# Kernel optimization log

Hardware: AMD Instinct MI355X
Metric: run time of the kernel (lower is better)

Reference implementation:

```python
import jax, jax.numpy as jnp
import numpy as np

K_FUTURE = 3
GAMMA = 0.25
LAMBDA_CP = 0.1
EPS = 1e-08


def setup_inputs() -> dict:
    key = jax.random.key(0)
    ks = jax.random.split(key, 8)
    B, T, d, Kc = 64, 512, 1024, 256
    Z = jax.random.normal(ks[0], (B, T, d), dtype=jnp.float32)
    # torch init: uniform(-1/Kc, 1/Kc)
    codebook = jax.random.uniform(ks[1], (Kc, d), dtype=jnp.float32,
                                  minval=-1.0 / Kc, maxval=1.0 / Kc)
    s = 1.0 / np.sqrt(d)
    gru_Wih = jax.random.normal(ks[2], (3 * d, d), dtype=jnp.float32) * s
    gru_Whh = jax.random.normal(ks[3], (3 * d, d), dtype=jnp.float32) * s
    gru_bih = jnp.zeros((3 * d,), jnp.float32)
    gru_bhh = jnp.zeros((3 * d,), jnp.float32)
    proj_W = jax.random.normal(ks[4], (d, d), dtype=jnp.float32) * s
    proj_b = jnp.zeros((d,), jnp.float32)
    return {"Z": Z, "codebook": codebook, "gru_Wih": gru_Wih, "gru_Whh": gru_Whh,
            "gru_bih": gru_bih, "gru_bhh": gru_bhh, "proj_W": proj_W, "proj_b": proj_b}


def _gru(x, Wih, Whh, bih, bhh):
    # x: (B, T, d) -> hidden states (B, T, d); torch GRU gate math
    B, T, d = x.shape

    def step(h, xt):
        gi = xt @ Wih.T + bih
        gh = h @ Whh.T + bhh
        i_r, i_z, i_n = jnp.split(gi, 3, axis=-1)
        h_r, h_z, h_n = jnp.split(gh, 3, axis=-1)
        r = jax.nn.sigmoid(i_r + h_r)
        z = jax.nn.sigmoid(i_z + h_z)
        n = jnp.tanh(i_n + r * h_n)
        h_new = (1.0 - z) * n + z * h
        return h_new, h_new

    h0 = jnp.zeros((B, d), x.dtype)
    _, hs = jax.lax.scan(step, h0, jnp.swapaxes(x, 0, 1))
    return jnp.swapaxes(hs, 0, 1)


def _quantize(Z, codebook):
    B, T, d = Z.shape
    flat = Z.reshape(-1, d)                                   # (N, d)
    # squared euclidean distances; argmin identical to cdist(p=2)
    d2 = (jnp.sum(flat * flat, axis=1, keepdims=True)
          - 2.0 * flat @ codebook.T
          + jnp.sum(codebook * codebook, axis=1)[None, :])    # (N, Kc)
    idx = jnp.argmin(d2, axis=1)                              # (N,)
    quantized = codebook[idx].reshape(B, T, d)
    return quantized, idx.reshape(B, T)


def _context_loss(Z, quantized, gru_Wih, gru_Whh, gru_bih, gru_bhh, proj_W, proj_b):
    B, T, d = Z.shape
    hs = _gru(quantized, gru_Wih, gru_Whh, gru_bih, gru_bhh)
    h = hs @ proj_W.T + proj_b                                # (B, T, d)
    total = jnp.float32(0.0)
    for k in range(1, K_FUTURE + 1):
        if T <= k:
            continue
        hk = h[:, :T - k]                                     # (B, T-k, d)
        zk = Z[:, k:]                                         # (B, T-k, d)
        pos = jnp.einsum('btd,btd->bt', hk, zk)               # (B, T-k)
        # sum over tau of mean over batch
        pos_loss = jnp.sum(jnp.mean(-jnp.log(jax.nn.sigmoid(pos) + EPS), axis=0))
        # negatives use a random batch permutation; the mean over (b, c) is
        # permutation-invariant, so compute the full pairwise logits.
        neg = jnp.einsum('btd,ctd->tbc', hk, zk)              # (T-k, B, B)
        neg_loss = jnp.sum(jnp.mean(-jnp.log(1.0 - jax.nn.sigmoid(neg) + EPS), axis=(1, 2)))
        total = total + pos_loss + LAMBDA_CP * neg_loss
    if K_FUTURE > 0 and T > K_FUTURE:
        total = total / (K_FUTURE * (T - K_FUTURE))
    return total


def _vq_loss(Z, quantized):
    commitment = jnp.mean((jax.lax.stop_gradient(Z) - quantized) ** 2)
    codebook_l = jnp.mean((Z - jax.lax.stop_gradient(quantized)) ** 2)
    return commitment + GAMMA * codebook_l


def reference(Z, codebook, gru_Wih, gru_Whh, gru_bih, gru_bhh, proj_W, proj_b):
    quantized, indices = _quantize(Z, codebook)
    L_cp = _context_loss(Z, quantized, gru_Wih, gru_Whh, gru_bih, gru_bhh, proj_W, proj_b)
    L_vq = _vq_loss(Z, quantized)
    L_total = L_cp + L_vq
    return quantized, indices, L_total, L_cp, L_vq
```

## Files before the change

### kernel.cpp

```cpp
#include <hip/hip_runtime.h>
#include <hip/hip_bf16.h>

#define B_ 64
#define T_ 512
#define D_ 1024
#define NQ_ (B_*T_*D_)
#define NI_ (B_*T_)

typedef __attribute__((ext_vector_type(8))) short bf16x8;
typedef __attribute__((ext_vector_type(4))) float f32x4;

__device__ inline ushort f2bf(float f) {
    uint x = __float_as_uint(f);
    return (ushort)((x + 0x7FFFu + ((x >> 16) & 1u)) >> 16);
}
__device__ inline float bf2f(ushort u) { return __uint_as_float(((uint)u) << 16); }

__device__ __forceinline__ void astore(ushort* p, ushort v) {
    __hip_atomic_store(p, v, __ATOMIC_RELAXED, __HIP_MEMORY_SCOPE_AGENT);
}

typedef const __attribute__((address_space(1))) void GV;
typedef __attribute__((address_space(3))) void LV;
__device__ __forceinline__ void gll16(const void* g, void* l) {
    __builtin_amdgcn_global_load_lds((GV*)g, (LV*)l, 16, 0, 0);
}

__device__ __forceinline__ float sigf(float x) { return 1.0f / (1.0f + __expf(-x)); }
__device__ __forceinline__ float tanhfast(float x) {
    float e = __expf(-2.0f * fabsf(x));
    float t = (1.0f - e) / (1.0f + e);
    return copysignf(t, x);
}

__global__ __launch_bounds__(256) void conv_kernel(const float* __restrict__ src,
                                                   ushort* __restrict__ dst, int n) {
    int i = (blockIdx.x * 256 + threadIdx.x) * 4;
    if (i >= n) return;
    float4 v = *reinterpret_cast<const float4*>(src + i);
    ushort4 o;
    o.x = f2bf(v.x); o.y = f2bf(v.y); o.z = f2bf(v.z); o.w = f2bf(v.w);
    *reinterpret_cast<ushort4*>(dst + i) = o;
}

__global__ __launch_bounds__(256) void whhfr_kernel(const float* __restrict__ Whh,
                                                    ushort* __restrict__ Whh_fr) {
    int l = threadIdx.x & 63;
    int unit = blockIdx.x * 4 + (threadIdx.x >> 6);
    int c = unit & 31;
    int g = (unit >> 5) % 3;
    int jb = unit / 96;
    int row = g * 1024 + jb * 16 + (l & 15);
    int k0 = c * 32 + (l >> 4) * 8;
    const float* s = Whh + (size_t)row * 1024 + k0;
    float4 f0 = *reinterpret_cast<const float4*>(s);
    float4 f1 = *reinterpret_cast<const float4*>(s + 4);
    uint4 pk;
    pk.x = (uint)f2bf(f0.x) | ((uint)f2bf(f0.y) << 16);
    pk.y = (uint)f2bf(f0.z) | ((uint)f2bf(f0.w) << 16);
    pk.z = (uint)f2bf(f1.x) | ((uint)f2bf(f1.y) << 16);
    pk.w = (uint)f2bf(f1.z) | ((uint)f2bf(f1.w) << 16);
    reinterpret_cast<uint4*>(Whh_fr)[(size_t)unit * 64 + l] = pk;
}

__device__ inline float np_pairwise_sq_1024(const float* a) {
    float L[8];
    for (int c = 0; c < 8; ++c) {
        const float* p = a + c * 128;
        float r[8];
        #pragma unroll
        for (int k = 0; k < 8; ++k) r[k] = __fmul_rn(p[k], p[k]);
        for (int i = 8; i < 128; i += 8) {
            #pragma unroll
            for (int k = 0; k < 8; ++k) {
                float v = p[i + k];
                r[k] = __fadd_rn(r[k], __fmul_rn(v, v));
            }
        }
        L[c] = __fadd_rn(__fadd_rn(__fadd_rn(r[0], r[1]), __fadd_rn(r[2], r[3])),
                         __fadd_rn(__fadd_rn(r[4], r[5]), __fadd_rn(r[6], r[7])));
    }
    return __fadd_rn(__fadd_rn(__fadd_rn(L[0], L[1]), __fadd_rn(L[2], L[3])),
                     __fadd_rn(__fadd_rn(L[4], L[5]), __fadd_rn(L[6], L[7])));
}

__global__ __launch_bounds__(256) void c2_kernel(const float* __restrict__ cb,
                                                 float* __restrict__ c2) {
    int j = threadIdx.x;
    c2[j] = np_pairwise_sq_1024(cb + (size_t)j * D_);
}

__global__ __launch_bounds__(256) void quantize_kernel(const float* __restrict__ Z,
                                                       const float* __restrict__ cb,
                                                       const float* __restrict__ c2,
                                                       float* __restrict__ qout,
                                                       float* __restrict__ idxout,
                                                       int* __restrict__ idxT) {
    __shared__ float rows[8][D_];
    __shared__ float z2s[8];
    __shared__ float d2s[256];
    __shared__ int   idxs[256];
    __shared__ int   bestIdx[8];
    int tid = threadIdx.x;
    size_t row0 = (size_t)blockIdx.x * 8;

    for (int p = 0; p < 8; ++p) {
        float4 v = *reinterpret_cast<const float4*>(Z + (row0 + p) * D_ + tid * 4);
        *reinterpret_cast<float4*>(&rows[p][tid * 4]) = v;
    }
    __syncthreads();

    if (tid < 8) z2s[tid] = np_pairwise_sq_1024(rows[tid]);

    float g2[8];
    #pragma unroll
    for (int r = 0; r < 8; ++r) g2[r] = 0.0f;
    const float* crow = cb + (size_t)tid * D_;
    for (int e = 0; e < D_; e += 4) {
        float4 cv = *reinterpret_cast<const float4*>(crow + e);
        #pragma unroll
        for (int r = 0; r < 8; ++r) {
            g2[r] = __fmaf_rn(__fmul_rn(2.0f, rows[r][e]),     cv.x, g2[r]);
            g2[r] = __fmaf_rn(__fmul_rn(2.0f, rows[r][e + 1]), cv.y, g2[r]);
            g2[r] = __fmaf_rn(__fmul_rn(2.0f, rows[r][e + 2]), cv.z, g2[r]);
            g2[r] = __fmaf_rn(__fmul_rn(2.0f, rows[r][e + 3]), cv.w, g2[r]);
        }
    }
    __syncthreads();

    for (int r = 0; r < 8; ++r) {
        d2s[tid] = __fadd_rn(__fsub_rn(z2s[r], g2[r]), c2[tid]);
        idxs[tid] = tid;
        __syncthreads();
        for (int s = 128; s > 0; s >>= 1) {
            if (tid < s) {
                float ov = d2s[tid + s]; int oi = idxs[tid + s];
                if (ov < d2s[tid] || (ov == d2s[tid] && oi < idxs[tid])) {
                    d2s[tid] = ov; idxs[tid] = oi;
                }
            }
            __syncthreads();
        }
        if (tid == 0) bestIdx[r] = idxs[0];
        __syncthreads();
    }

    if (tid < 8) {
        int row = (int)row0 + tid;
        idxout[row] = (float)bestIdx[tid];
        idxT[((row & 511) << 6) + (row >> 9)] = bestIdx[tid];
    }
    for (int r = 0; r < 8; ++r) {
        int bi = bestIdx[r];
        float4 v = *reinterpret_cast<const float4*>(cb + (size_t)bi * D_ + tid * 4);
        *reinterpret_cast<float4*>(qout + (row0 + r) * D_ + tid * 4) = v;
    }
}

__global__ __launch_bounds__(256) void gmat_kernel(const float* __restrict__ cb,
                                                   const float* __restrict__ Wih,
                                                   const float* __restrict__ bih,
                                                   const float* __restrict__ bhh,
                                                   ushort* __restrict__ Gp) {
    int m0 = blockIdx.x * 64;
    int n0 = blockIdx.y * 64;
    __shared__ ushort As[64][136];
    __shared__ ushort Bs[64][136];
    int tid = threadIdx.x;
    int w = tid >> 6, l = tid & 63, lr = l & 15, lk = l >> 4;
    f32x4 acc[4];
    #pragma unroll
    for (int i = 0; i < 4; ++i) acc[i] = f32x4{0.f, 0.f, 0.f, 0.f};

    for (int kc = 0; kc < D_; kc += 128) {
        for (int v = tid; v < 2048; v += 256) {
            int r = (v >> 4) & 63, kp = (v & 15) << 3;
            const float* src = (v < 1024) ? (cb  + (size_t)(m0 + r) * D_ + kc + kp)
                                          : (Wih + (size_t)(n0 + r) * D_ + kc + kp);
            float4 f0 = *reinterpret_cast<const float4*>(src);
            float4 f1 = *reinterpret_cast<const float4*>(src + 4);
            uint4 pk;
            pk.x = (uint)f2bf(f0.x) | ((uint)f2bf(f0.y) << 16);
            pk.y = (uint)f2bf(f0.z) | ((uint)f2bf(f0.w) << 16);
            pk.z = (uint)f2bf(f1.x) | ((uint)f2bf(f1.y) << 16);
            pk.w = (uint)f2bf(f1.z) | ((uint)f2bf(f1.w) << 16);
            ushort* dst = (v < 1024) ? &As[r][kp] : &Bs[r][kp];
            *reinterpret_cast<uint4*>(dst) = pk;
        }
        __syncthreads();
        #pragma unroll
        for (int kk = 0; kk < 4; ++kk) {
            bf16x8 bb = *reinterpret_cast<const bf16x8*>(&Bs[(w << 4) + lr][(kk << 5) + (lk << 3)]);
            #pragma unroll
            for (int mi = 0; mi < 4; ++mi) {
                bf16x8 a = *reinterpret_cast<const bf16x8*>(&As[(mi << 4) + lr][(kk << 5) + (lk << 3)]);
                acc[mi] = __builtin_amdgcn_mfma_f32_16x16x32_bf16(a, bb, acc[mi], 0, 0, 0);
            }
        }
        __syncthreads();
    }
    int n = n0 + (w << 4) + lr;
    int gate = n >> 10, jj = n & 1023;
    float bias = bih[n] + (gate < 2 ? bhh[n] : 0.0f);
    #pragma unroll
    for (int mi = 0; mi < 4; ++mi)
        #pragma unroll
        for (int reg = 0; reg < 4; ++reg) {
            int m = m0 + (mi << 4) + (lk << 2) + reg;
            Gp[((((size_t)m << 10) | jj) << 2) + gate] = f2bf(acc[mi][reg] + bias);
        }
}

__global__ __launch_bounds__(256, 1) void recur_kernel(
    const ushort* __restrict__ Whh_fr,
    const ushort* __restrict__ Gp,
    const int*    __restrict__ idxT,
    const float*  __restrict__ bhh,
    ushort* h_hist,
    uint*   flags)
{
    extern __shared__ ushort dynlds[];
    const int tid = threadIdx.x, blk = blockIdx.x;
    const int w = tid >> 6, l = tid & 63;
    const int lr = l & 15, lk = l >> 4;
    const int j0 = blk << 4, j = j0 + lr;
    const int b_base = (w << 4) + (lk << 2);
    const float bhhn = bhh[2048 + j];
    const ushort* Bbase = Whh_fr + (size_t)blk * 49152;
    ushort* myfrag = dynlds + (w << 14);
    const int rowoff = (((w << 4) + lr) << 10) + (lk << 3);
    float hfp[4] = {0.f, 0.f, 0.f, 0.f};
    bool dead = false;

    bf16x8 Bfr[96];
    #pragma unroll
    for (int c = 0; c < 32; ++c) {
        Bfr[c]      = *reinterpret_cast<const bf16x8*>(Bbase +         (c << 9) + (l << 3));
        Bfr[32 + c] = *reinterpret_cast<const bf16x8*>(Bbase + 16384 + (c << 9) + (l << 3));
        Bfr[64 + c] = *reinterpret_cast<const bf16x8*>(Bbase + 32768 + (c << 9) + (l << 3));
    }

    for (int t = 0; t < T_; ++t) {
        const ushort* src = h_hist + ((size_t)(t == 0 ? 512 : t - 1) << 16) + rowoff;
        #pragma unroll
        for (int c = 0; c < 32; ++c)
            gll16(src + (c << 5), myfrag + (c << 9));
        __syncthreads();

        f32x4 acc0 = {0.f,0.f,0.f,0.f}, acc1 = acc0, acc2 = acc0;
        #pragma unroll
        for (int c = 0; c < 32; ++c) {
            bf16x8 a = *reinterpret_cast<const bf16x8*>(myfrag + (c << 9) + (l << 3));
            acc0 = __builtin_amdgcn_mfma_f32_16x16x32_bf16(a, Bfr[c],      acc0, 0, 0, 0);
            acc1 = __builtin_amdgcn_mfma_f32_16x16x32_bf16(a, Bfr[32 + c], acc1, 0, 0, 0);
            acc2 = __builtin_amdgcn_mfma_f32_16x16x32_bf16(a, Bfr[64 + c], acc2, 0, 0, 0);
        }

        ushort* hw = h_hist + ((size_t)t << 16);
        const uint4 it4 = *reinterpret_cast<const uint4*>(idxT + (t << 6) + b_base);
        const int* itp = (const int*)&it4;
        #pragma unroll
        for (int reg = 0; reg < 4; ++reg) {
            const int b = b_base + reg;
            const ushort4 g4 = *reinterpret_cast<const ushort4*>(Gp + ((((size_t)itp[reg] << 10) | j) << 2));
            float rr = sigf(bf2f(g4.x) + acc0[reg]);
            float zz = sigf(bf2f(g4.y) + acc1[reg]);
            float nn = tanhfast(bf2f(g4.z) + rr * (acc2[reg] + bhhn));
            float hn = (1.0f - zz) * nn + zz * hfp[reg];
            hfp[reg] = hn;
            astore(&hw[(b << 10) + j], f2bf(hn));
        }

        if (t < T_ - 1) {
            __syncthreads();
            if (tid == 0)
                __hip_atomic_store(&flags[blk << 4], (uint)(t + 1),
                                   __ATOMIC_RELAXED, __HIP_MEMORY_SCOPE_AGENT);
            if (!dead) {
                uint spins = 0;
                while (__hip_atomic_load(&flags[(tid & 63) << 4], __ATOMIC_RELAXED,
                                         __HIP_MEMORY_SCOPE_AGENT) < (uint)(t + 1)) {
                    if (++spins > (1u << 20)) { dead = true; break; }
                }
            }
            __syncthreads();
        }
    }
}

__global__ __launch_bounds__(256) void proj_gemm_kernel(const ushort* __restrict__ h_hist,
                                                        const ushort* __restrict__ projW_bf,
                                                        const float* __restrict__ projb,
                                                        ushort* __restrict__ hproj,
                                                        int ch) {
    int t = ch * 256 + blockIdx.x;
    int n0 = blockIdx.y * 64;
    __shared__ ushort As[64][136];
    __shared__ ushort Bs[64][136];
    int tid = threadIdx.x;
    int w = tid >> 6, l = tid & 63, lr = l & 15, lk = l >> 4;
    f32x4 acc[4];
    #pragma unroll
    for (int i = 0; i < 4; ++i) acc[i] = f32x4{0.f,0.f,0.f,0.f};

    for (int kc = 0; kc < D_; kc += 128) {
        for (int v = tid; v < 2048; v += 256) {
            int r = (v >> 4) & 63, kp = (v & 15) << 3;
            if (v < 1024)
                *reinterpret_cast<uint4*>(&As[r][kp]) =
                    *reinterpret_cast<const uint4*>(h_hist + ((size_t)t << 16) + ((size_t)r << 10) + kc + kp);
            else
                *reinterpret_cast<uint4*>(&Bs[r][kp]) =
                    *reinterpret_cast<const uint4*>(projW_bf + ((size_t)(n0 + r) << 10) + kc + kp);
        }
        __syncthreads();
        #pragma unroll
        for (int kk = 0; kk < 4; ++kk) {
            bf16x8 bb = *reinterpret_cast<const bf16x8*>(&Bs[(w << 4) + lr][(kk << 5) + (lk << 3)]);
            #pragma unroll
            for (int mi = 0; mi < 4; ++mi) {
                bf16x8 a = *reinterpret_cast<const bf16x8*>(&As[(mi << 4) + lr][(kk << 5) + (lk << 3)]);
                acc[mi] = __builtin_amdgcn_mfma_f32_16x16x32_bf16(a, bb, acc[mi], 0, 0, 0);
            }
        }
        __syncthreads();
    }
    int n = n0 + (w << 4) + lr;
    float pb = projb[n];
    #pragma unroll
    for (int mi = 0; mi < 4; ++mi)
        #pragma unroll
        for (int reg = 0; reg < 4; ++reg) {
            int b = (mi << 4) + (lk << 2) + reg;
            hproj[((size_t)(t & 255) << 16) + (b << 10) + n] = f2bf(acc[mi][reg] + pb);
        }
}

__global__ __launch_bounds__(256) void cpc_loss_kernel(const ushort* __restrict__ hproj,
                                                       const float* __restrict__ Z,
                                                       double* __restrict__ cp_sum,
                                                       int ch) {
    int tp = ch * 256 + blockIdx.x;
    int k = blockIdx.y + 1;
    if (tp >= T_ - k) return;
    __shared__ float Hs[64][33];
    __shared__ float Zs[64][33];
    int tid = threadIdx.x;
    int tx = tid & 15, ty = tid >> 4;
    float acc[4][4] = {};
    const ushort* Hbase = hproj + ((size_t)(tp & 255) << 16);
    const float* Zbase = Z + (size_t)(tp + k) * D_;
    const size_t zstride = (size_t)T_ * D_;
    int r = tid >> 3, c = (tid & 7) << 2;

    for (int kc = 0; kc < D_; kc += 32) {
        #pragma unroll
        for (int p = 0; p < 2; ++p) {
            int rr2 = r + 32 * p;
            ushort4 hv = *reinterpret_cast<const ushort4*>(Hbase + (size_t)rr2 * D_ + kc + c);
            float4 zv = *reinterpret_cast<const float4*>(Zbase + (size_t)rr2 * zstride + kc + c);
            Hs[rr2][c] = bf2f(hv.x); Hs[rr2][c+1] = bf2f(hv.y);
            Hs[rr2][c+2] = bf2f(hv.z); Hs[rr2][c+3] = bf2f(hv.w);
            Zs[rr2][c] = zv.x; Zs[rr2][c+1] = zv.y; Zs[rr2][c+2] = zv.z; Zs[rr2][c+3] = zv.w;
        }
        __syncthreads();
        #pragma unroll
        for (int kk = 0; kk < 32; ++kk) {
            float av[4], bv[4];
            #pragma unroll
            for (int i = 0; i < 4; ++i) av[i] = Hs[ty + 16*i][kk];
            #pragma unroll
            for (int jv = 0; jv < 4; ++jv) bv[jv] = Zs[tx + 16*jv][kk];
            #pragma unroll
            for (int i = 0; i < 4; ++i)
                #pragma unroll
                for (int jv = 0; jv < 4; ++jv)
                    acc[i][jv] = __fmaf_rn(av[i], bv[jv], acc[i][jv]);
        }
        __syncthreads();
    }

    double lsum = 0.0;
    #pragma unroll
    for (int i = 0; i < 4; ++i) {
        #pragma unroll
        for (int jv = 0; jv < 4; ++jv) {
            int bb = ty + 16*i, cc2 = tx + 16*jv;
            double v = (double)acc[i][jv];
            double sg = 1.0 / (1.0 + exp(-v));
            lsum += (0.1 / 4096.0) * (-log(1.0 - sg + 1e-8));
            if (bb == cc2) lsum += (1.0 / 64.0) * (-log(sg + 1e-8));
        }
    }
    __shared__ double red[256];
    red[tid] = lsum; __syncthreads();
    for (int s2 = 128; s2 > 0; s2 >>= 1) {
        if (tid < s2) red[tid] += red[tid + s2];
        __syncthreads();
    }
    if (tid == 0) atomicAdd(cp_sum, red[0]);
}

__global__ __launch_bounds__(256) void vq_kernel(const float* __restrict__ Z,
                                                 const float* __restrict__ Q,
                                                 double* __restrict__ vq_sum) {
    size_t i0 = ((size_t)blockIdx.x * 256 + threadIdx.x) * 4;
    const size_t stride = (size_t)2048 * 256 * 4;
    double s = 0.0;
    for (size_t i = i0; i < (size_t)NQ_; i += stride) {
        float4 z = *reinterpret_cast<const float4*>(Z + i);
        float4 q = *reinterpret_cast<const float4*>(Q + i);
        double d0 = (double)z.x - (double)q.x;
        double d1 = (double)z.y - (double)q.y;
        double d2 = (double)z.z - (double)q.z;
        double d3 = (double)z.w - (double)q.w;
        s += d0*d0 + d1*d1 + d2*d2 + d3*d3;
    }
    __shared__ double red[256];
    int tid = threadIdx.x;
    red[tid] = s; __syncthreads();
    for (int k = 128; k > 0; k >>= 1) {
        if (tid < k) red[tid] += red[tid + k];
        __syncthreads();
    }
    if (tid == 0) atomicAdd(vq_sum, red[0]);
}

__global__ void finalize_kernel(const double* __restrict__ accum,
                                float* __restrict__ scal) {
    double cp = accum[0] / 1527.0;
    double vq = accum[1] * 1.25 / (double)NQ_;
    scal[0] = (float)(cp + vq);
    scal[1] = (float)cp;
    scal[2] = (float)vq;
}

extern "C" void kernel_launch(void* const* d_in, const int* in_sizes, int n_in,
                              void* d_out, int out_size, void* d_ws, size_t ws_size,
                              hipStream_t stream) {
    const float* Z     = (const float*)d_in[0];
    const float* cb    = (const float*)d_in[1];
    const float* Wih   = (const float*)d_in[2];
    const float* Whh   = (const float*)d_in[3];
    const float* bih   = (const float*)d_in[4];
    const float* bhh   = (const float*)d_in[5];
    const float* projW = (const float*)d_in[6];
    const float* projb = (const float*)d_in[7];

    float* out       = (float*)d_out;
    float* quantized = out;
    float* idxout    = out + (size_t)NQ_;
    float* scal      = out + (size_t)NQ_ + NI_;

    char* p = (char*)d_ws;
    ushort* Whh_fr   = (ushort*)p;  p += 6291456;
    ushort* projW_bf = (ushort*)p;  p += 2097152;
    ushort* Gp       = (ushort*)p;  p += 2097152;
    int*    idxT     = (int*)p;     p += 131072;
    float*  c2f      = (float*)p;   p += 4096;
    char*   ctrl     = p;           p += 8192;
    ushort* h_hist   = (ushort*)p;  p += (size_t)513 * 131072;
    ushort* hproj    = (ushort*)p;  p += (size_t)256 * 131072;

    uint*   flags = (uint*)ctrl;
    double* accum = (double*)(ctrl + 4096);

    hipMemsetAsync(ctrl, 0, 8192, stream);
    hipMemsetAsync(h_hist + ((size_t)512 << 16), 0, 131072, stream);

    conv_kernel<<<1024, 256, 0, stream>>>(projW, projW_bf, 1048576);
    whhfr_kernel<<<1536, 256, 0, stream>>>(Whh, Whh_fr);
    c2_kernel<<<1, 256, 0, stream>>>(cb, c2f);
    quantize_kernel<<<4096, 256, 0, stream>>>(Z, cb, c2f, quantized, idxout, idxT);
    gmat_kernel<<<dim3(4, 48), 256, 0, stream>>>(cb, Wih, bih, bhh, Gp);

    hipFuncSetAttribute(reinterpret_cast<const void*>(recur_kernel),
                        hipFuncAttributeMaxDynamicSharedMemorySize, 131072);
    recur_kernel<<<dim3(64), dim3(256), 131072, stream>>>(Whh_fr, Gp, idxT, bhh,
                                                          h_hist, flags);

    for (int ch = 0; ch < 2; ++ch) {
        proj_gemm_kernel<<<dim3(256, 16), 256, 0, stream>>>(h_hist, projW_bf, projb, hproj, ch);
        cpc_loss_kernel<<<dim3(256, 3), 256, 0, stream>>>(hproj, Z, &accum[0], ch);
    }

    vq_kernel<<<2048, 256, 0, stream>>>(Z, quantized, &accum[1]);
    finalize_kernel<<<1, 1, 0, stream>>>(accum, scal);
}
```

Baseline: 5.932 ms.

## Stream Whh fragments per step, transpose MFMA operands, vectorize h stores, single-wave spin

The recurrent GRU kernel no longer keeps 96 bf16x8 Whh fragments resident in registers. It reloads them from global or L2 on every timestep, with the MFMA operands swapped so each lane owns one batch row and four hidden columns. That layout lets the gate preactivations be fetched with two 16-byte loads and the new hidden state written as one 64-bit atomic store instead of four 16-bit stores. The grid-wide flag spin is limited to wave 0, uses __all, and adds a dummy FMA loop during the wait. The change trades register pressure for re-streaming about 96KB of weights per block per step through the cache, which puts extra latency on the serial critical path. The __syncthreads before the MFMA loop was replaced by s_waitcnt vmcnt(0) plus a sched_barrier, yet each wave reads only its own LDS region.

```diff
diff --git a/kernel.cpp b/kernel.cpp
--- a/kernel.cpp
+++ b/kernel.cpp
@@ -16,7 +16,7 @@
 }
 __device__ inline float bf2f(ushort u) { return __uint_as_float(((uint)u) << 16); }
 
-__device__ __forceinline__ void astore(ushort* p, ushort v) {
+__device__ __forceinline__ void astore64(ulong* p, ulong v) {
     __hip_atomic_store(p, v, __ATOMIC_RELAXED, __HIP_MEMORY_SCOPE_AGENT);
 }
 
@@ -223,63 +223,75 @@
     const int tid = threadIdx.x, blk = blockIdx.x;
     const int w = tid >> 6, l = tid & 63;
     const int lr = l & 15, lk = l >> 4;
-    const int j0 = blk << 4, j = j0 + lr;
-    const int b_base = (w << 4) + (lk << 2);
-    const float bhhn = bhh[2048 + j];
+    const int j0 = blk << 4;
+    const int b  = (w << 4) + lr;
+    const int jq = j0 + (lk << 2);
     const ushort* Bbase = Whh_fr + (size_t)blk * 49152;
     ushort* myfrag = dynlds + (w << 14);
     const int rowoff = (((w << 4) + lr) << 10) + (lk << 3);
+    const float4 bhhn4 = *reinterpret_cast<const float4*>(&bhh[2048 + jq]);
+    const float* bhhn = (const float*)&bhhn4;
     float hfp[4] = {0.f, 0.f, 0.f, 0.f};
     bool dead = false;
 
-    bf16x8 Bfr[96];
-    #pragma unroll
-    for (int c = 0; c < 32; ++c) {
-        Bfr[c]      = *reinterpret_cast<const bf16x8*>(Bbase +         (c << 9) + (l << 3));
-        Bfr[32 + c] = *reinterpret_cast<const bf16x8*>(Bbase + 16384 + (c << 9) + (l << 3));
-        Bfr[64 + c] = *reinterpret_cast<const bf16x8*>(Bbase + 32768 + (c << 9) + (l << 3));
-    }
-
     for (int t = 0; t < T_; ++t) {
         const ushort* src = h_hist + ((size_t)(t == 0 ? 512 : t - 1) << 16) + rowoff;
         #pragma unroll
         for (int c = 0; c < 32; ++c)
             gll16(src + (c << 5), myfrag + (c << 9));
-        __syncthreads();
+
+        const int ci = idxT[(t << 6) + b];
+        const uint4* gpv = reinterpret_cast<const uint4*>(Gp + ((((size_t)ci << 10) | jq) << 2));
+        uint4 ga = gpv[0], gb2 = gpv[1];
+        ushort gp16[16];
+        *reinterpret_cast<uint4*>(&gp16[0]) = ga;
+        *reinterpret_cast<uint4*>(&gp16[8]) = gb2;
+
+        asm volatile("s_waitcnt vmcnt(0)" ::: "memory");
+        __builtin_amdgcn_sched_barrier(0);
 
         f32x4 acc0 = {0.f,0.f,0.f,0.f}, acc1 = acc0, acc2 = acc0;
-        #pragma unroll
+        #pragma unroll 8
         for (int c = 0; c < 32; ++c) {
-            bf16x8 a = *reinterpret_cast<const bf16x8*>(myfrag + (c << 9) + (l << 3));
-            acc0 = __builtin_amdgcn_mfma_f32_16x16x32_bf16(a, Bfr[c],      acc0, 0, 0, 0);
-            acc1 = __builtin_amdgcn_mfma_f32_16x16x32_bf16(a, Bfr[32 + c], acc1, 0, 0, 0);
-            acc2 = __builtin_amdgcn_mfma_f32_16x16x32_bf16(a, Bfr[64 + c], acc2, 0, 0, 0);
-        }
-
-        ushort* hw = h_hist + ((size_t)t << 16);
-        const uint4 it4 = *reinterpret_cast<const uint4*>(idxT + (t << 6) + b_base);
-        const int* itp = (const int*)&it4;
+            bf16x8 hfr = *reinterpret_cast<const bf16x8*>(myfrag + (c << 9) + (l << 3));
+            bf16x8 w0 = *reinterpret_cast<const bf16x8*>(Bbase +         (c << 9) + (l << 3));
+            bf16x8 w1 = *reinterpret_cast<const bf16x8*>(Bbase + 16384 + (c << 9) + (l << 3));
+            bf16x8 w2 = *reinterpret_cast<const bf16x8*>(Bbase + 32768 + (c << 9) + (l << 3));
+            acc0 = __builtin_amdgcn_mfma_f32_16x16x32_bf16(w0, hfr, acc0, 0, 0, 0);
+            acc1 = __builtin_amdgcn_mfma_f32_16x16x32_bf16(w1, hfr, acc1, 0, 0, 0);
+            acc2 = __builtin_amdgcn_mfma_f32_16x16x32_bf16(w2, hfr, acc2, 0, 0, 0);
+        }
+
+        ushort4 hs;
+        ushort* hsp = (ushort*)&hs;
         #pragma unroll
         for (int reg = 0; reg < 4; ++reg) {
-            const int b = b_base + reg;
-            const ushort4 g4 = *reinterpret_cast<const ushort4*>(Gp + ((((size_t)itp[reg] << 10) | j) << 2));
-            float rr = sigf(bf2f(g4.x) + acc0[reg]);
-            float zz = sigf(bf2f(g4.y) + acc1[reg]);
-            float nn = tanhfast(bf2f(g4.z) + rr * (acc2[reg] + bhhn));
+            float rr = sigf(bf2f(gp16[reg * 4 + 0]) + acc0[reg]);
+            float zz = sigf(bf2f(gp16[reg * 4 + 1]) + acc1[reg]);
+            float nn = tanhfast(bf2f(gp16[reg * 4 + 2]) + rr * (acc2[reg] + bhhn[reg]));
             float hn = (1.0f - zz) * nn + zz * hfp[reg];
             hfp[reg] = hn;
-            astore(&hw[(b << 10) + j], f2bf(hn));
-        }
+            hsp[reg] = f2bf(hn);
+        }
+        astore64(reinterpret_cast<ulong*>(h_hist + ((size_t)t << 16) + (b << 10) + jq),
+                 *reinterpret_cast<ulong*>(&hs));
 
         if (t < T_ - 1) {
             __syncthreads();
             if (tid == 0)
                 __hip_atomic_store(&flags[blk << 4], (uint)(t + 1),
                                    __ATOMIC_RELAXED, __HIP_MEMORY_SCOPE_AGENT);
-            if (!dead) {
+            if (w == 0 && !dead) {
                 uint spins = 0;
-                while (__hip_atomic_load(&flags[(tid & 63) << 4], __ATOMIC_RELAXED,
-                                         __HIP_MEMORY_SCOPE_AGENT) < (uint)(t + 1)) {
+                float pump = 1.0f;
+                for (;;) {
+                    uint f = __hip_atomic_load(&flags[l << 4], __ATOMIC_RELAXED,
+                                               __HIP_MEMORY_SCOPE_AGENT);
+                    if (__all(f >= (uint)(t + 1))) break;
+                    #pragma unroll
+                    for (int q = 0; q < 16; ++q)
+                        pump = __fmaf_rn(pump, 1.0000001f, 0.0000001f);
+                    asm volatile("" :: "v"(pump));
                     if (++spins > (1u << 20)) { dead = true; break; }
                 }
             }
```

After: 6.925 ms. 16.7% more time.
